# Kernel optimization log

Hardware: AMD Instinct MI355X
Metric: run time of the kernel (lower is better)

Reference implementation:

```python
import jax, jax.numpy as jnp
import numpy as np

NEG = -1e9  # stands in for -inf in masked_fill; identical softmax output, grad-safe


def _sfu(inputs, fusion, Wr, Wg):
    # SFU: m = [x, f, x*f, x-f]; o = relu(m@Wr)*g + (1-g)*x, g = sigmoid(m@Wg)
    m = jnp.concatenate([inputs, fusion, inputs * fusion, inputs - fusion], axis=-1)
    x = jax.nn.relu(m @ Wr)
    g = jax.nn.sigmoid(m @ Wg)
    return x * g + (1.0 - g) * inputs


def _stage(U, V, cmask, qmask, E, B, p):
    # One Aligner stage = InterAlign followed by SelfAlign. Batch-first layout (b, len, d).
    Wu, bu, Wv, bv, Wri, Wgi, gi, W1, b1, W2, b2, Wrs, Wgs, gs = p
    # ---- InterAlign ----
    Ct = jax.nn.relu(U @ Wu + bu)              # (b, c, d)
    Qt = jax.nn.relu(V @ Wv + bv)              # (b, q, d)
    E0 = jnp.einsum('bcd,bqd->bcq', Ct, Qt)    # (b, c, q)
    if E is not None:
        Es = jax.nn.softmax(jnp.where(cmask[:, :, None] == 0, NEG, E), axis=1)   # softmax over c
        Bs = jax.nn.softmax(jnp.where(cmask[:, None, :] == 0, NEG, B), axis=2)   # softmax over c (cols)
        E = E0 + gi * jnp.einsum('bce,beq->bcq', Bs, Es)
    else:
        E = E0
    Ett = jax.nn.softmax(jnp.where(qmask[:, None, :] == 0, NEG, E), axis=2)
    qctx = jnp.einsum('bcq,bqd->bcd', Ett, V)  # attend question
    h = _sfu(U, qctx, Wri, Wgi)
    # ---- SelfAlign ----
    H1 = jax.nn.relu(h @ W1 + b1)
    H2 = jax.nn.relu(h @ W2 + b2)
    B0 = jnp.einsum('bcd,bed->bce', H1, H2)    # (b, c, c)
    if B is not None:
        B1s = jax.nn.softmax(jnp.where(cmask[:, :, None] == 0, NEG, B), axis=1)
        B2s = jax.nn.softmax(jnp.where(cmask[:, None, :] == 0, NEG, B), axis=2)
        B = B0 + gs * jnp.einsum('bce,bef->bcf', B2s, B1s)
    else:
        B = B0
    c = U.shape[1]
    B = B * (1.0 - jnp.eye(c, dtype=B.dtype))[None]  # masked_fill_(eye, 0.0): zero diagonal
    Btt = jax.nn.softmax(jnp.where(cmask[:, None, :] == 0, NEG, B), axis=2)
    hctx = jnp.einsum('bce,bed->bcd', Btt, h)
    Z = _sfu(h, hctx, Wrs, Wgs)
    return Z, E, B


def setup_inputs() -> dict:
    key = jax.random.key(0)
    b, c_len, q_len, d = 8, 768, 96, 768
    T = 2  # number of aligner stages
    ks = jax.random.split(key, 16)
    s = 0.02
    inp = {
        'U': jax.random.normal(ks[0], (b, c_len, d), jnp.float32),
        'V': jax.random.normal(ks[1], (b, q_len, d), jnp.float32),
        'U_mask': jax.random.randint(ks[2], (b, c_len), 0, 2).astype(jnp.int32),
        'V_mask': jax.random.randint(ks[3], (b, q_len), 0, 2).astype(jnp.int32),
        'Wu': jax.random.normal(ks[4], (T, d, d), jnp.float32) * s,
        'bu': jnp.zeros((T, d), jnp.float32),
        'Wv': jax.random.normal(ks[5], (T, d, d), jnp.float32) * s,
        'bv': jnp.zeros((T, d), jnp.float32),
        'Wr_i': jax.random.normal(ks[6], (T, 4 * d, d), jnp.float32) * s,
        'Wg_i': jax.random.normal(ks[7], (T, 4 * d, d), jnp.float32) * s,
        'gamma_i': jnp.full((T,), 3.0, jnp.float32),
        'W1': jax.random.normal(ks[8], (T, d, d), jnp.float32) * s,
        'b1': jnp.zeros((T, d), jnp.float32),
        'W2': jax.random.normal(ks[9], (T, d, d), jnp.float32) * s,
        'b2': jnp.zeros((T, d), jnp.float32),
        'Wr_s': jax.random.normal(ks[10], (T, 4 * d, d), jnp.float32) * s,
        'Wg_s': jax.random.normal(ks[11], (T, 4 * d, d), jnp.float32) * s,
        'gamma_s': jnp.full((T,), 3.0, jnp.float32),
    }
    return inp


def reference(U, V, U_mask, V_mask, Wu, bu, Wv, bv, Wr_i, Wg_i, gamma_i,
              W1, b1, W2, b2, Wr_s, Wg_s, gamma_s):
    E = None
    B = None
    x = U
    for t in range(Wu.shape[0]):  # fixed small stage loop (align_1 -> align_2)
        p = (Wu[t], bu[t], Wv[t], bv[t], Wr_i[t], Wg_i[t], gamma_i[t],
             W1[t], b1[t], W2[t], b2[t], Wr_s[t], Wg_s[t], gamma_s[t])
        x, E, B = _stage(x, V, U_mask, V_mask, E, B, p)
    return x
```

## Files before the change

kernel.cpp:

```cpp
#include <hip/hip_runtime.h>
#include <math.h>

#define NEGV -1e9f

typedef short bf16x8 __attribute__((ext_vector_type(8)));
typedef float f32x4 __attribute__((ext_vector_type(4)));
typedef unsigned short ushort8v __attribute__((ext_vector_type(8)));

static __device__ __forceinline__ unsigned short f2bf(float f) {
  unsigned int u = __float_as_uint(f);
  unsigned int r = (u + 0x7fffu + ((u >> 16) & 1u)) >> 16;
  return (unsigned short)r;
}

static __device__ __forceinline__ int xcd_swz(int lin, int nwg) {
  int q = nwg >> 3, r = nwg & 7;
  int x = lin & 7, i = lin >> 3;
  return (x < r) ? x * (q + 1) + i : r * (q + 1) + (x - r) * q + i;
}

__device__ __forceinline__ float wred_max(float v) {
  #pragma unroll
  for (int o = 32; o > 0; o >>= 1) v = fmaxf(v, __shfl_down(v, o, 64));
  return v;
}
__device__ __forceinline__ float wred_sum(float v) {
  #pragma unroll
  for (int o = 32; o > 0; o >>= 1) v += __shfl_down(v, o, 64);
  return v;
}

__global__ __launch_bounds__(256)
void softmax_row_mask(const float* __restrict__ X, const int* __restrict__ mask,
                      float* __restrict__ Y, unsigned short* __restrict__ Ybf,
                      int R, int Cn)
{
  int bz = blockIdx.y, r = blockIdx.x, tid = threadIdx.x;
  const float* xr = X + ((size_t)bz * R + r) * Cn;
  const int*   mr = mask + (size_t)bz * Cn;
  float*       yr = Y ? (Y + ((size_t)bz * R + r) * Cn) : nullptr;
  unsigned short* yb = Ybf ? (Ybf + ((size_t)bz * R + r) * Cn) : nullptr;
  __shared__ float sred[4];

  float mx = -INFINITY;
  for (int i = tid; i < Cn; i += 256) {
    float v = (mr[i] != 0) ? xr[i] : NEGV;
    mx = fmaxf(mx, v);
  }
  float wm = wred_max(mx);
  if ((tid & 63) == 0) sred[tid >> 6] = wm;
  __syncthreads();
  mx = fmaxf(fmaxf(sred[0], sred[1]), fmaxf(sred[2], sred[3]));
  __syncthreads();

  float s = 0.f;
  for (int i = tid; i < Cn; i += 256) {
    float v = (mr[i] != 0) ? xr[i] : NEGV;
    s += expf(v - mx);
  }
  float wsv = wred_sum(s);
  if ((tid & 63) == 0) sred[tid >> 6] = wsv;
  __syncthreads();
  s = sred[0] + sred[1] + sred[2] + sred[3];
  float inv = 1.0f / s;

  for (int i = tid; i < Cn; i += 256) {
    float v = (mr[i] != 0) ? xr[i] : NEGV;
    float o = expf(v - mx) * inv;
    if (yr) yr[i] = o;
    if (yb) yb[i] = f2bf(o);
  }
}

__global__ __launch_bounds__(256)
void transp_f32(const float* __restrict__ X, float* __restrict__ Y,
                int R, int C, long sX, long sY)
{
  int bz = blockIdx.z;
  X += (size_t)bz * sX;
  Y += (size_t)bz * sY;
  __shared__ float T[64][65];
  int c0 = blockIdx.x * 64, r0 = blockIdx.y * 64;
  int t = threadIdx.x;
  int tr = t >> 4, tc4 = (t & 15) * 4;
  #pragma unroll
  for (int rr = 0; rr < 4; ++rr) {
    int r = tr + rr * 16;
    float4 v = make_float4(0.f, 0.f, 0.f, 0.f);
    if (c0 + tc4 < C)
      v = *reinterpret_cast<const float4*>(X + (size_t)(r0 + r) * C + c0 + tc4);
    T[r][tc4 + 0] = v.x; T[r][tc4 + 1] = v.y;
    T[r][tc4 + 2] = v.z; T[r][tc4 + 3] = v.w;
  }
  __syncthreads();
  #pragma unroll
  for (int rr = 0; rr < 4; ++rr) {
    int cc = tr + rr * 16;
    int gc = c0 + cc;
    if (gc < C) {
      float4 o = make_float4(T[tc4 + 0][cc], T[tc4 + 1][cc], T[tc4 + 2][cc], T[tc4 + 3][cc]);
      *reinterpret_cast<float4*>(Y + (size_t)gc * R + r0 + tc4) = o;
    }
  }
}

__global__ __launch_bounds__(256)
void transpV(const float* __restrict__ V, unsigned short* __restrict__ VT)
{
  int bz = blockIdx.z;
  const float* Vb = V + (size_t)bz * 96 * 768;
  unsigned short* Yb = VT + (size_t)bz * 768 * 96;
  __shared__ float T[64][65];
  int c0 = blockIdx.x * 64, r0 = blockIdx.y * 64;
  int t = threadIdx.x;
  int tr = t >> 4, tc4 = (t & 15) * 4;
  #pragma unroll
  for (int rr = 0; rr < 4; ++rr) {
    int r = tr + rr * 16;
    int gr = r0 + r;
    float4 v = make_float4(0.f, 0.f, 0.f, 0.f);
    if (gr < 96)
      v = *reinterpret_cast<const float4*>(Vb + (size_t)gr * 768 + c0 + tc4);
    T[r][tc4 + 0] = v.x; T[r][tc4 + 1] = v.y;
    T[r][tc4 + 2] = v.z; T[r][tc4 + 3] = v.w;
  }
  __syncthreads();
  #pragma unroll
  for (int rr = 0; rr < 4; ++rr) {
    int cc = tr + rr * 16;
    int gc = c0 + cc;
    #pragma unroll
    for (int e = 0; e < 4; ++e) {
      int gr = r0 + tc4 + e;
      if (gr < 96) Yb[(size_t)gc * 96 + gr] = f2bf(T[tc4 + e][cc]);
    }
  }
}

__global__ __launch_bounds__(256)
void concat_bf16(const float* __restrict__ X, const float* __restrict__ F,
                 unsigned short* __restrict__ Mc)
{
  int idx = blockIdx.x * 256 + threadIdx.x;
  int m  = idx / 96;
  int kk = (idx - m * 96) * 8;
  const float* xp = X + (size_t)m * 768 + kk;
  const float* fp = F + (size_t)m * 768 + kk;
  float4 a0 = *reinterpret_cast<const float4*>(xp);
  float4 a1 = *reinterpret_cast<const float4*>(xp + 4);
  float4 b0 = *reinterpret_cast<const float4*>(fp);
  float4 b1 = *reinterpret_cast<const float4*>(fp + 4);
  float xa[8] = {a0.x, a0.y, a0.z, a0.w, a1.x, a1.y, a1.z, a1.w};
  float fa[8] = {b0.x, b0.y, b0.z, b0.w, b1.x, b1.y, b1.z, b1.w};
  ushort8v o0, o1, o2;
  #pragma unroll
  for (int i = 0; i < 8; ++i) {
    o0[i] = f2bf(xa[i]);
    o1[i] = f2bf(fa[i]);
    o2[i] = f2bf(xa[i] * fa[i]);
  }
  unsigned short* base = Mc + (size_t)m * 2304 + kk;
  *reinterpret_cast<ushort8v*>(base)        = o0;
  *reinterpret_cast<ushort8v*>(base +  768) = o1;
  *reinterpret_cast<ushort8v*>(base + 1536) = o2;
}

__global__ __launch_bounds__(256)
void transp_cast4(const float* __restrict__ W0, const float* __restrict__ W1a,
                  const float* __restrict__ W2a, const float* __restrict__ W3a,
                  unsigned short* __restrict__ Wt)
{
  int z = blockIdx.z;
  const float* W = (z == 0) ? W0 : (z == 1) ? W1a : (z == 2) ? W2a : W3a;
  unsigned short* Y = Wt + (size_t)z * 768 * 768;
  __shared__ float T[64][65];
  int n0 = blockIdx.x * 64, k0 = blockIdx.y * 64;
  int t = threadIdx.x;
  int tr = t >> 4, tc4 = (t & 15) * 4;
  #pragma unroll
  for (int r = 0; r < 4; ++r) {
    int k = tr + r * 16;
    float4 v = *reinterpret_cast<const float4*>(W + (size_t)(k0 + k) * 768 + n0 + tc4);
    T[k][tc4 + 0] = v.x; T[k][tc4 + 1] = v.y; T[k][tc4 + 2] = v.z; T[k][tc4 + 3] = v.w;
  }
  __syncthreads();
  #pragma unroll
  for (int r = 0; r < 4; ++r) {
    int n = tr + r * 16;
    ushort4 o;
    o.x = f2bf(T[tc4 + 0][n]); o.y = f2bf(T[tc4 + 1][n]);
    o.z = f2bf(T[tc4 + 2][n]); o.w = f2bf(T[tc4 + 3][n]);
    *reinterpret_cast<ushort4*>(Y + (size_t)(n0 + n) * 768 + k0 + tc4) = o;
  }
}

__global__ __launch_bounds__(256)
void transp_cast2(const float* __restrict__ Wa, const float* __restrict__ Wb,
                  unsigned short* __restrict__ Wt)
{
  const float* W = blockIdx.z ? Wb : Wa;
  unsigned short* Y = Wt + (size_t)blockIdx.z * 768 * 2304;
  __shared__ float T[64][65];
  int n0 = blockIdx.x * 64, k0 = blockIdx.y * 64;
  int t = threadIdx.x;
  int tr = t >> 4, tc4 = (t & 15) * 4;
  #pragma unroll
  for (int r = 0; r < 4; ++r) {
    int k = tr + r * 16;
    int gk = k0 + k;
    float4 v = *reinterpret_cast<const float4*>(W + (size_t)gk * 768 + n0 + tc4);
    if (gk < 768) {
      float4 u = *reinterpret_cast<const float4*>(W + (size_t)(gk + 2304) * 768 + n0 + tc4);
      v.x += u.x; v.y += u.y; v.z += u.z; v.w += u.w;
    } else if (gk < 1536) {
      float4 u = *reinterpret_cast<const float4*>(W + (size_t)(gk + 1536) * 768 + n0 + tc4);
      v.x -= u.x; v.y -= u.y; v.z -= u.z; v.w -= u.w;
    }
    T[k][tc4 + 0] = v.x; T[k][tc4 + 1] = v.y; T[k][tc4 + 2] = v.z; T[k][tc4 + 3] = v.w;
  }
  __syncthreads();
  #pragma unroll
  for (int r = 0; r < 4; ++r) {
    int n = tr + r * 16;
    ushort4 o;
    o.x = f2bf(T[tc4 + 0][n]); o.y = f2bf(T[tc4 + 1][n]);
    o.z = f2bf(T[tc4 + 2][n]); o.w = f2bf(T[tc4 + 3][n]);
    *reinterpret_cast<ushort4*>(Y + (size_t)(n0 + n) * 2304 + k0 + tc4) = o;
  }
}

__global__ __launch_bounds__(256)
void transp_cast(const float* __restrict__ W, unsigned short* __restrict__ Wt,
                 int K, long sW, long sWt)
{
  int bz = blockIdx.z;
  W  += (size_t)bz * sW;
  Wt += (size_t)bz * sWt;
  __shared__ float T[64][65];
  int n0 = blockIdx.x * 64, k0 = blockIdx.y * 64;
  int t = threadIdx.x;
  int tr = t >> 4, tc4 = (t & 15) * 4;
  #pragma unroll
  for (int r = 0; r < 4; ++r) {
    int k = tr + r * 16;
    float4 v = *reinterpret_cast<const float4*>(W + (size_t)(k0 + k) * 768 + n0 + tc4);
    T[k][tc4 + 0] = v.x; T[k][tc4 + 1] = v.y; T[k][tc4 + 2] = v.z; T[k][tc4 + 3] = v.w;
  }
  __syncthreads();
  #pragma unroll
  for (int r = 0; r < 4; ++r) {
    int n = tr + r * 16;
    ushort4 o;
    o.x = f2bf(T[tc4 + 0][n]); o.y = f2bf(T[tc4 + 1][n]);
    o.z = f2bf(T[tc4 + 2][n]); o.w = f2bf(T[tc4 + 3][n]);
    *reinterpret_cast<ushort4*>(Wt + (size_t)(n0 + n) * K + k0 + tc4) = o;
  }
}

__global__ __launch_bounds__(256)
void cast_bf16(const float* __restrict__ X, unsigned short* __restrict__ Y, int n8)
{
  int idx = blockIdx.x * 256 + threadIdx.x;
  if (idx >= n8) return;
  float4 a0 = *reinterpret_cast<const float4*>(X + (size_t)idx * 8);
  float4 a1 = *reinterpret_cast<const float4*>(X + (size_t)idx * 8 + 4);
  ushort8v o;
  o[0] = f2bf(a0.x); o[1] = f2bf(a0.y); o[2] = f2bf(a0.z); o[3] = f2bf(a0.w);
  o[4] = f2bf(a1.x); o[5] = f2bf(a1.y); o[6] = f2bf(a1.z); o[7] = f2bf(a1.w);
  *reinterpret_cast<ushort8v*>(Y + (size_t)idx * 8) = o;
}


template<int NB, int WAVES>
__global__ __launch_bounds__(64 * WAVES)
void mfma_gemm(const unsigned short* __restrict__ A,
               const unsigned short* __restrict__ Bt0,
               const unsigned short* __restrict__ Bt1,
               const float* __restrict__ bias0, const float* __restrict__ bias1,
               const float* __restrict__ alphap, const float* __restrict__ C0,
               float* __restrict__ F0, float* __restrict__ F1,
               unsigned short* __restrict__ O0, unsigned short* __restrict__ O1,
               int M, int N, int K,
               long sA, long sB, long sC0, long sC,
               int relu, int zerodiag)
{
  const int RG = WAVES / 4;
  const int TM = RG * 48;
  __shared__ unsigned short As[2][TM * 32];
  __shared__ unsigned short Bs0[2][2048];
  __shared__ unsigned short Bs1[2][NB == 2 ? 2048 : 16];

  int nx = gridDim.x, ny = gridDim.y;
  int nwg = nx * ny * gridDim.z;
  int lin = blockIdx.x + nx * (blockIdx.y + ny * blockIdx.z);
  int sw = xcd_swz(lin, nwg);
  int bxi = sw % nx; int rest = sw / nx;
  int byi = rest % ny; int bz = rest / ny;

  A   += (size_t)bz * sA;
  Bt0 += (size_t)bz * sB;
  if (NB == 2) Bt1 += (size_t)bz * sB;
  const float* C0b = C0 ? (C0 + (size_t)bz * sC0) : nullptr;

  int tid = threadIdx.x;
  int w = tid >> 6, l = tid & 63;
  int m0 = byi * TM, n0 = bxi * 64;
  int wr = w >> 2, wc = w & 3;

  int g8 = (((l & 3) ^ ((l >> 3) & 3))) * 8;
  int rowA = w * 16 + (l >> 2); if (rowA > TM - 1) rowA = TM - 1;
  int rB = n0 + (w & 3) * 16 + (l >> 2); if (rB > N - 1) rB = N - 1;
  const unsigned short* srcA  = A + (size_t)(m0 + rowA) * K + g8;
  const unsigned short* srcB0 = Bt0 + (size_t)rB * K + g8;
  const unsigned short* srcB1 = (NB == 2) ? Bt1 + (size_t)rB * K + g8 : nullptr;

#define GG_STAGE(kt, bi) do { int kk0 = (kt) * 32;                                                                        \
    if (w < TM / 16)                                                                                                      \
      __builtin_amdgcn_global_load_lds((const unsigned int*)(srcA + kk0),  (unsigned int*)&As[bi][0]  + w * 256, 16, 0, 0); \
    if (w < 4)                                                                                                            \
      __builtin_amdgcn_global_load_lds((const unsigned int*)(srcB0 + kk0), (unsigned int*)&Bs0[bi][0] + w * 256, 16, 0, 0); \
    if (NB == 2 && w >= 4)                                                                                                \
      __builtin_amdgcn_global_load_lds((const unsigned int*)(srcB1 + kk0), (unsigned int*)&Bs1[bi][0] + (w - 4) * 256, 16, 0, 0); \
  } while (0)

  f32x4 a0[3] = {};
  f32x4 a1v[3] = {};

  const int NT = K / 32;
  int prm = ((l >> 4) ^ ((l >> 1) & 3)) * 8;
  GG_STAGE(0, 0);
  __syncthreads();
  int cur = 0;
  for (int kt = 0; kt < NT; ++kt) {
    if (kt + 1 < NT) GG_STAGE(kt + 1, cur ^ 1);

    bf16x8 af[3];
    #pragma unroll
    for (int i = 0; i < 3; ++i) {
      int off = (wr * 48 + i * 16 + (l & 15)) * 32 + prm;
      af[i] = *reinterpret_cast<const bf16x8*>(&As[cur][off]);
    }
    int offB = (wc * 16 + (l & 15)) * 32 + prm;
    bf16x8 b0 = *reinterpret_cast<const bf16x8*>(&Bs0[cur][offB]);
    #pragma unroll
    for (int i = 0; i < 3; ++i)
      a0[i] = __builtin_amdgcn_mfma_f32_16x16x32_bf16(af[i], b0, a0[i], 0, 0, 0);
    if (NB == 2) {
      bf16x8 b1 = *reinterpret_cast<const bf16x8*>(&Bs1[cur][offB]);
      #pragma unroll
      for (int i = 0; i < 3; ++i)
        a1v[i] = __builtin_amdgcn_mfma_f32_16x16x32_bf16(af[i], b1, a1v[i], 0, 0, 0);
    }
    __syncthreads();
    cur ^= 1;
  }
#undef GG_STAGE

  float alpha = alphap ? alphap[0] : 1.0f;
  float* F0b = F0 ? F0 + (size_t)bz * sC : nullptr;
  float* F1b = F1 ? F1 + (size_t)bz * sC : nullptr;
  unsigned short* O0b = O0 ? O0 + (size_t)bz * sC : nullptr;
  unsigned short* O1b = O1 ? O1 + (size_t)bz * sC : nullptr;

  #pragma unroll
  for (int i = 0; i < 3; ++i) {
    #pragma unroll
    for (int qq = 0; qq < 4; ++qq) {
      int gm = m0 + wr * 48 + i * 16 + (l >> 4) * 4 + qq;
      int gn = n0 + wc * 16 + (l & 15);
      if (gn >= N) continue;
      size_t oidx = (size_t)gm * N + gn;
      float v = alpha * a0[i][qq];
      if (bias0) v += bias0[gn];
      if (relu) v = fmaxf(v, 0.f);
      if (C0b) v += C0b[oidx];
      if (zerodiag && gm == gn) v = 0.f;
      if (F0b) F0b[oidx] = v;
      if (O0b) O0b[oidx] = f2bf(v);
      if (NB == 2) {
        float v1 = alpha * a1v[i][qq];
        if (bias1) v1 += bias1[gn];
        if (relu) v1 = fmaxf(v1, 0.f);
        if (F1b) F1b[oidx] = v1;
        if (O1b) O1b[oidx] = f2bf(v1);
      }
    }
  }
}

__global__ __launch_bounds__(512)
void sfu_mfma(const unsigned short* __restrict__ Mc,
              const unsigned short* __restrict__ Brt,
              const unsigned short* __restrict__ Bgt,
              const float* __restrict__ Xres, float* __restrict__ Z,
              unsigned short* __restrict__ Zb)
{
  __shared__ unsigned short As[2][3072];
  __shared__ unsigned short Brs[2][2048];
  __shared__ unsigned short Bgs[2][2048];
  const int K = 2304;
  const int NT = 72;

  int nx = gridDim.x, ny = gridDim.y;
  int nwg = nx * ny;
  int lin = blockIdx.x + nx * blockIdx.y;
  int sw = xcd_swz(lin, nwg);
  int bxi = sw % nx; int byi = sw / nx;

  int tid = threadIdx.x;
  int w = tid >> 6, l = tid & 63;
  int m0 = byi * 96, n0 = bxi * 64;
  int wr = w >> 2, wc = w & 3;

  int g8 = (((l & 3) ^ ((l >> 3) & 3))) * 8;
  int rowA = w * 16 + (l >> 2); if (rowA > 95) rowA = 95;
  int rB = n0 + (w & 3) * 16 + (l >> 2);
  const unsigned short* srcA = Mc  + (size_t)(m0 + rowA) * K + g8;
  const unsigned short* srcR = Brt + (size_t)rB * K + g8;
  const unsigned short* srcG = Bgt + (size_t)rB * K + g8;

#define SFU_STAGE(kt, bi) do { int kk0 = (kt) * 32;                                                                      \
    if (w < 6)                                                                                                           \
      __builtin_amdgcn_global_load_lds((const unsigned int*)(srcA + kk0), (unsigned int*)&As[bi][0]  + w * 256, 16, 0, 0); \
    if (w < 4)                                                                                                           \
      __builtin_amdgcn_global_load_lds((const unsigned int*)(srcR + kk0), (unsigned int*)&Brs[bi][0] + w * 256, 16, 0, 0); \
    if (w >= 4)                                                                                                          \
      __builtin_amdgcn_global_load_lds((const unsigned int*)(srcG + kk0), (unsigned int*)&Bgs[bi][0] + (w - 4) * 256, 16, 0, 0); \
  } while (0)

  f32x4 aR[3] = {};
  f32x4 aG[3] = {};

  int prm = ((l >> 4) ^ ((l >> 1) & 3)) * 8;
  SFU_STAGE(0, 0);
  __syncthreads();
  int cur = 0;
  for (int kt = 0; kt < NT; ++kt) {
    if (kt + 1 < NT) SFU_STAGE(kt + 1, cur ^ 1);

    bf16x8 af[3];
    #pragma unroll
    for (int i = 0; i < 3; ++i) {
      int off = (wr * 48 + i * 16 + (l & 15)) * 32 + prm;
      af[i] = *reinterpret_cast<const bf16x8*>(&As[cur][off]);
    }
    int offB = (wc * 16 + (l & 15)) * 32 + prm;
    bf16x8 br = *reinterpret_cast<const bf16x8*>(&Brs[cur][offB]);
    bf16x8 bg = *reinterpret_cast<const bf16x8*>(&Bgs[cur][offB]);
    #pragma unroll
    for (int i = 0; i < 3; ++i) {
      aR[i] = __builtin_amdgcn_mfma_f32_16x16x32_bf16(af[i], br, aR[i], 0, 0, 0);
      aG[i] = __builtin_amdgcn_mfma_f32_16x16x32_bf16(af[i], bg, aG[i], 0, 0, 0);
    }
    __syncthreads();
    cur ^= 1;
  }
#undef SFU_STAGE

  #pragma unroll
  for (int i = 0; i < 3; ++i) {
    #pragma unroll
    for (int qq = 0; qq < 4; ++qq) {
      int gm = m0 + wr * 48 + i * 16 + (l >> 4) * 4 + qq;
      int gn = n0 + wc * 16 + (l & 15);
      float r = fmaxf(aR[i][qq], 0.f);
      float g = 1.0f / (1.0f + expf(-aG[i][qq]));
      float xv = Xres[(size_t)gm * 768 + gn];
      float z = r * g + (1.0f - g) * xv;
      Z[(size_t)gm * 768 + gn] = z;
      if (Zb) Zb[(size_t)gm * 768 + gn] = f2bf(z);
    }
  }
}

static void launch_mfma1(const unsigned short* A, const unsigned short* Bt,
                         const float* bias, const float* alphap, const float* C0,
                         float* F0, unsigned short* O0,
                         int M, int N, int K, long sA, long sB, long sC0, long sC,
                         int relu, int zd, int batch, int tm, hipStream_t s)
{
  dim3 g((N + 63) / 64, M / tm, batch);
  if (tm == 48)
    mfma_gemm<1, 4><<<g, 256, 0, s>>>(A, Bt, nullptr, bias, nullptr, alphap, C0,
                                      F0, nullptr, O0, nullptr, M, N, K, sA, sB, sC0, sC, relu, zd);
  else
    mfma_gemm<1, 8><<<g, 512, 0, s>>>(A, Bt, nullptr, bias, nullptr, alphap, C0,
                                      F0, nullptr, O0, nullptr, M, N, K, sA, sB, sC0, sC, relu, zd);
}

static void launch_mfma2(const unsigned short* A, const unsigned short* Bt0,
                         const unsigned short* Bt1, const float* bias0, const float* bias1,
                         unsigned short* O0, unsigned short* O1,
                         int M, int N, int K, long sA, long sB,
                         int relu, int batch, hipStream_t s)
{
  dim3 g((N + 63) / 64, M / 96, batch);
  mfma_gemm<2, 8><<<g, 512, 0, s>>>(A, Bt0, Bt1, bias0, bias1, nullptr, nullptr,
                                    nullptr, nullptr, O0, O1, M, N, K, sA, sB, 0, sA,
                                    relu, 0);
}

static void launch_sfu(const float* x, const float* f, const float* Wr, const float* Wg,
                       const float* xres, float* z, unsigned short* zb,
                       unsigned short* Mc, unsigned short* Wt, hipStream_t s)
{
  concat_bf16<<<dim3(2304), 256, 0, s>>>(x, f, Mc);
  unsigned short* Wrt = Wt;
  unsigned short* Wgt = Wt + (size_t)768 * 2304;
  transp_cast2<<<dim3(12, 36, 2), 256, 0, s>>>(Wr, Wg, Wt);
  sfu_mfma<<<dim3(12, 64), 512, 0, s>>>(Mc, Wrt, Wgt, xres, z, zb);
}

extern "C" void kernel_launch(void* const* d_in, const int* in_sizes, int n_in,
                              void* d_out, int out_size, void* d_ws, size_t ws_size,
                              hipStream_t stream)
{
  const int b = 8, c = 768, q = 96, d = 768, T = 2;
  const float* U   = (const float*)d_in[0];
  const float* V   = (const float*)d_in[1];
  const int*   Um  = (const int*)d_in[2];
  const int*   Vm  = (const int*)d_in[3];
  const float* Wu  = (const float*)d_in[4];
  const float* bu  = (const float*)d_in[5];
  const float* Wv  = (const float*)d_in[6];
  const float* bv  = (const float*)d_in[7];
  const float* Wri = (const float*)d_in[8];
  const float* Wgi = (const float*)d_in[9];
  const float* gi  = (const float*)d_in[10];
  const float* W1  = (const float*)d_in[11];
  const float* b1  = (const float*)d_in[12];
  const float* W2  = (const float*)d_in[13];
  const float* b2  = (const float*)d_in[14];
  const float* Wrs = (const float*)d_in[15];
  const float* Wgs = (const float*)d_in[16];
  const float* gs  = (const float*)d_in[17];
  float* out = (float*)d_out;

  const size_t big = (size_t)b * c * d;
  const size_t smE = (size_t)b * c * q;
  float* ws   = (float*)d_ws;
  float* xbuf = ws + 0 * big;
  float* h    = ws + 1 * big;
  float* Bm   = ws + 2 * big;
  float* t1   = ws + 3 * big;
  float* t2   = ws + 4 * big;
  float* t3   = ws + 5 * big;
  float* t4   = ws + 6 * big;
  float* Ebuf = ws + 7 * big;
  float* E0b  = Ebuf + smE;
  float* Esb  = E0b + smE;
  float* spare = Esb + smE;
  float* slotE = spare + smE;
  float* WTf  = slotE + big / 2;

  unsigned short* Mc  = (unsigned short*)t1;
  unsigned short* Wt  = (unsigned short*)t4;
  unsigned short* t1h = (unsigned short*)t1;
  unsigned short* t3h = (unsigned short*)t3;
  unsigned short* t3h2 = t3h + big;
  unsigned short* slotEb = (unsigned short*)slotE;
  unsigned short* H1b = t1h;
  unsigned short* H2b = H1b + big;
  unsigned short* WuT = (unsigned short*)WTf;
  unsigned short* WvT  = WuT  + (size_t)d * d;
  unsigned short* W1T  = WvT  + (size_t)d * d;
  unsigned short* W2T  = W1T  + (size_t)d * d;
  unsigned short* Vb16 = W2T  + (size_t)d * d;
  unsigned short* Qtbb = Vb16 + smE;
  unsigned short* VTb  = Qtbb + smE;
  unsigned short* EsTb = VTb  + smE;
  unsigned short* Ettb = EsTb + smE;

  const long cd = (long)c * d, cq = (long)c * q, qd = (long)q * d, cc = (long)c * c;
  const size_t dd = (size_t)d * d;
  const int cast_big = (int)(big / 8);
  (void)ws_size; (void)spare;

  const float* x = U;
  for (int t = 0; t < T; ++t) {
    const float* Writ = Wri + (size_t)t * 4 * dd;
    const float* Wgit = Wgi + (size_t)t * 4 * dd;
    const float* Wrst = Wrs + (size_t)t * 4 * dd;
    const float* Wgst = Wgs + (size_t)t * 4 * dd;

    transp_cast4<<<dim3(12, 12, 4), 256, 0, stream>>>(Wu + t * dd, Wv + t * dd,
                                                      W1 + t * dd, W2 + t * dd, WuT);
    if (t == 0) {
      cast_bf16<<<dim3((int)(smE / 8 / 256)), 256, 0, stream>>>(V, Vb16, (int)(smE / 8));
      transpV<<<dim3(12, 2, b), 256, 0, stream>>>(V, VTb);
      cast_bf16<<<dim3(cast_big / 256), 256, 0, stream>>>(x, t3h, cast_big);
    }

    launch_mfma1(t3h, WuT, bu + t * d, nullptr, nullptr, nullptr, t1h,
                 b * c, d, d, 0, 0, 0, 0, 1, 0, 1, 96, stream);
    launch_mfma1(Vb16, WvT, bv + t * d, nullptr, nullptr, nullptr, Qtbb,
                 b * q, d, d, 0, 0, 0, 0, 1, 0, 1, 48, stream);
    float* e0dst = (t == 0) ? Ebuf : E0b;
    launch_mfma1(t1h, Qtbb, nullptr, nullptr, nullptr, e0dst, nullptr,
                 c, q, d, cd, qd, 0, cq, 0, 0, b, 48, stream);
    if (t > 0) {
      transp_f32<<<dim3(2, 12, b), 256, 0, stream>>>(Ebuf, Esb, c, q, cq, cq);
      softmax_row_mask<<<dim3(q, b), 256, 0, stream>>>(Esb, Um, nullptr, EsTb, q, c);
      softmax_row_mask<<<dim3(c, b), 256, 0, stream>>>(Bm, Um, nullptr, slotEb, c, c);
      launch_mfma1(slotEb, EsTb, nullptr, gi + t, E0b, Ebuf, nullptr,
                   c, q, c, cc, cq, cq, cq, 0, 0, b, 48, stream);
    }
    softmax_row_mask<<<dim3(c, b), 256, 0, stream>>>(Ebuf, Vm, nullptr, Ettb, c, q);
    launch_mfma1(Ettb, VTb, nullptr, nullptr, nullptr, t4, nullptr,
                 c, d, q, cq, qd, 0, cd, 0, 0, b, 96, stream);
    launch_sfu(x, t4, Writ, Wgit, x, h, t3h, Mc, Wt, stream);
    launch_mfma2(t3h, W1T, W2T, b1 + t * d, b2 + t * d, H1b, H2b,
                 b * c, d, d, 0, 0, 1, 1, stream);
    if (t == 0) {
      launch_mfma1(H1b, H2b, nullptr, nullptr, nullptr, Bm, nullptr,
                   c, c, d, cd, cd, 0, cc, 0, 1, b, 96, stream);
    } else {
      launch_mfma1(H1b, H2b, nullptr, nullptr, nullptr, xbuf, nullptr,
                   c, c, d, cd, cd, 0, cc, 0, 0, b, 96, stream);
      transp_f32<<<dim3(12, 12, b), 256, 0, stream>>>(Bm, t1, c, c, cc, cc);
      softmax_row_mask<<<dim3(c, b), 256, 0, stream>>>(t1, Um, nullptr, t3h2, c, c);
      launch_mfma1(slotEb, t3h2, nullptr, gs + t, xbuf, Bm, nullptr,
                   c, c, c, cc, cc, cc, cc, 0, 1, b, 96, stream);
    }
    softmax_row_mask<<<dim3(c, b), 256, 0, stream>>>(Bm, Um, nullptr, t3h2, c, c);
    transp_cast<<<dim3(12, 12, b), 256, 0, stream>>>(h, slotEb, 768, cd, cd);
    launch_mfma1(t3h2, slotEb, nullptr, nullptr, nullptr, t4, nullptr,
                 c, d, c, cc, cd, 0, cd, 0, 0, b, 96, stream);
    float* zdst = (t == T - 1) ? out : xbuf;
    unsigned short* zb16 = (t == T - 1) ? nullptr : t3h;
    launch_sfu(h, t4, Wrst, Wgst, h, zdst, zb16, Mc, Wt, stream);

    x = xbuf;
  }
}
```

Baseline: 755.0 us.

## Split K across two wave groups with larger per-wave tiles and LDS reduction

In the 8-wave GEMM and SFU kernels, the waves form two groups that take alternating K tiles. Each wave now computes a 48x32 sub-tile instead of 48x16, so every A fragment feeds more MFMAs and fewer LDS reads are needed per MFMA. After the loop the partial sums from group 1 are reduced into group 0 through an LDS buffer, and group 0 writes the epilogue. The cost is more accumulator registers, extra LDS, extra barriers for the reduction, and each wave sitting idle on every other K step. The 4-wave GEMM path is split into its own specialized kernel with unchanged logic.

Measured after the change: 920.6 us. +21.9%, slower.

```diff
diff --git a/kernel.cpp b/kernel.cpp
--- a/kernel.cpp
+++ b/kernel.cpp
@@ -271,24 +271,23 @@
 }
 
 
-template<int NB, int WAVES>
-__global__ __launch_bounds__(64 * WAVES)
-void mfma_gemm(const unsigned short* __restrict__ A,
-               const unsigned short* __restrict__ Bt0,
-               const unsigned short* __restrict__ Bt1,
-               const float* __restrict__ bias0, const float* __restrict__ bias1,
-               const float* __restrict__ alphap, const float* __restrict__ C0,
-               float* __restrict__ F0, float* __restrict__ F1,
-               unsigned short* __restrict__ O0, unsigned short* __restrict__ O1,
-               int M, int N, int K,
-               long sA, long sB, long sC0, long sC,
-               int relu, int zerodiag)
-{
-  const int RG = WAVES / 4;
-  const int TM = RG * 48;
-  __shared__ unsigned short As[2][TM * 32];
+template<int NB>
+__global__ __launch_bounds__(512)
+void mfma_gemm8(const unsigned short* __restrict__ A,
+                const unsigned short* __restrict__ Bt0,
+                const unsigned short* __restrict__ Bt1,
+                const float* __restrict__ bias0, const float* __restrict__ bias1,
+                const float* __restrict__ alphap, const float* __restrict__ C0,
+                float* __restrict__ F0, float* __restrict__ F1,
+                unsigned short* __restrict__ O0, unsigned short* __restrict__ O1,
+                int M, int N, int K,
+                long sA, long sB, long sC0, long sC,
+                int relu, int zerodiag)
+{
+  __shared__ unsigned short As[2][3072];
   __shared__ unsigned short Bs0[2][2048];
   __shared__ unsigned short Bs1[2][NB == 2 ? 2048 : 16];
+  __shared__ float MP[12 * 256];
 
   int nx = gridDim.x, ny = gridDim.y;
   int nwg = nx * ny * gridDim.z;
@@ -304,18 +303,19 @@
 
   int tid = threadIdx.x;
   int w = tid >> 6, l = tid & 63;
-  int m0 = byi * TM, n0 = bxi * 64;
-  int wr = w >> 2, wc = w & 3;
+  int m0 = byi * 96, n0 = bxi * 64;
+  int grp = w >> 2, pos = w & 3;
+  int wr = pos >> 1, wc = pos & 1;
 
   int g8 = (((l & 3) ^ ((l >> 3) & 3))) * 8;
-  int rowA = w * 16 + (l >> 2); if (rowA > TM - 1) rowA = TM - 1;
+  int rowA = w * 16 + (l >> 2); if (rowA > 95) rowA = 95;
   int rB = n0 + (w & 3) * 16 + (l >> 2); if (rB > N - 1) rB = N - 1;
   const unsigned short* srcA  = A + (size_t)(m0 + rowA) * K + g8;
   const unsigned short* srcB0 = Bt0 + (size_t)rB * K + g8;
   const unsigned short* srcB1 = (NB == 2) ? Bt1 + (size_t)rB * K + g8 : nullptr;
 
 #define GG_STAGE(kt, bi) do { int kk0 = (kt) * 32;                                                                        \
-    if (w < TM / 16)                                                                                                      \
+    if (w < 6)                                                                                                            \
       __builtin_amdgcn_global_load_lds((const unsigned int*)(srcA + kk0),  (unsigned int*)&As[bi][0]  + w * 256, 16, 0, 0); \
     if (w < 4)                                                                                                            \
       __builtin_amdgcn_global_load_lds((const unsigned int*)(srcB0 + kk0), (unsigned int*)&Bs0[bi][0] + w * 256, 16, 0, 0); \
@@ -323,8 +323,8 @@
       __builtin_amdgcn_global_load_lds((const unsigned int*)(srcB1 + kk0), (unsigned int*)&Bs1[bi][0] + (w - 4) * 256, 16, 0, 0); \
   } while (0)
 
-  f32x4 a0[3] = {};
-  f32x4 a1v[3] = {};
+  f32x4 a0[2][3] = {};
+  f32x4 a1[2][3] = {};
 
   const int NT = K / 32;
   int prm = ((l >> 4) ^ ((l >> 1) & 3)) * 8;
@@ -334,10 +334,147 @@
   for (int kt = 0; kt < NT; ++kt) {
     if (kt + 1 < NT) GG_STAGE(kt + 1, cur ^ 1);
 
+    if ((kt & 1) == grp) {
+      bf16x8 af[3];
+      #pragma unroll
+      for (int i = 0; i < 3; ++i) {
+        int off = (wr * 48 + i * 16 + (l & 15)) * 32 + prm;
+        af[i] = *reinterpret_cast<const bf16x8*>(&As[cur][off]);
+      }
+      #pragma unroll
+      for (int j = 0; j < 2; ++j) {
+        int offB = (wc * 32 + j * 16 + (l & 15)) * 32 + prm;
+        bf16x8 b0 = *reinterpret_cast<const bf16x8*>(&Bs0[cur][offB]);
+        #pragma unroll
+        for (int i = 0; i < 3; ++i)
+          a0[j][i] = __builtin_amdgcn_mfma_f32_16x16x32_bf16(af[i], b0, a0[j][i], 0, 0, 0);
+        if (NB == 2) {
+          bf16x8 b1 = *reinterpret_cast<const bf16x8*>(&Bs1[cur][offB]);
+          #pragma unroll
+          for (int i = 0; i < 3; ++i)
+            a1[j][i] = __builtin_amdgcn_mfma_f32_16x16x32_bf16(af[i], b1, a1[j][i], 0, 0, 0);
+        }
+      }
+    }
+    __syncthreads();
+    cur ^= 1;
+  }
+#undef GG_STAGE
+
+  int slot = pos * 64 + l;
+  #pragma unroll
+  for (int rnd = 0; rnd < 2 * NB; ++rnd) {
+    f32x4* col = (rnd < 2) ? &a0[rnd][0] : &a1[rnd - 2][0];
+    if (grp == 1) {
+      #pragma unroll
+      for (int i = 0; i < 3; ++i)
+        #pragma unroll
+        for (int k = 0; k < 4; ++k)
+          MP[(i * 4 + k) * 256 + slot] = col[i][k];
+    }
+    __syncthreads();
+    if (grp == 0) {
+      #pragma unroll
+      for (int i = 0; i < 3; ++i)
+        #pragma unroll
+        for (int k = 0; k < 4; ++k)
+          col[i][k] += MP[(i * 4 + k) * 256 + slot];
+    }
+    __syncthreads();
+  }
+
+  if (grp != 0) return;
+
+  float alpha = alphap ? alphap[0] : 1.0f;
+  float* F0b = F0 ? F0 + (size_t)bz * sC : nullptr;
+  float* F1b = F1 ? F1 + (size_t)bz * sC : nullptr;
+  unsigned short* O0b = O0 ? O0 + (size_t)bz * sC : nullptr;
+  unsigned short* O1b = O1 ? O1 + (size_t)bz * sC : nullptr;
+
+  #pragma unroll
+  for (int j = 0; j < 2; ++j) {
+    #pragma unroll
+    for (int i = 0; i < 3; ++i) {
+      #pragma unroll
+      for (int qq = 0; qq < 4; ++qq) {
+        int gm = m0 + wr * 48 + i * 16 + (l >> 4) * 4 + qq;
+        int gn = n0 + wc * 32 + j * 16 + (l & 15);
+        if (gn >= N) continue;
+        size_t oidx = (size_t)gm * N + gn;
+        float v = alpha * a0[j][i][qq];
+        if (bias0) v += bias0[gn];
+        if (relu) v = fmaxf(v, 0.f);
+        if (C0b) v += C0b[oidx];
+        if (zerodiag && gm == gn) v = 0.f;
+        if (F0b) F0b[oidx] = v;
+        if (O0b) O0b[oidx] = f2bf(v);
+        if (NB == 2) {
+          float v1 = alpha * a1[j][i][qq];
+          if (bias1) v1 += bias1[gn];
+          if (relu) v1 = fmaxf(v1, 0.f);
+          if (F1b) F1b[oidx] = v1;
+          if (O1b) O1b[oidx] = f2bf(v1);
+        }
+      }
+    }
+  }
+}
+
+__global__ __launch_bounds__(256)
+void mfma_gemm4(const unsigned short* __restrict__ A,
+                const unsigned short* __restrict__ Bt0,
+                const float* __restrict__ bias0,
+                const float* __restrict__ alphap, const float* __restrict__ C0,
+                float* __restrict__ F0, unsigned short* __restrict__ O0,
+                int M, int N, int K,
+                long sA, long sB, long sC0, long sC,
+                int relu, int zerodiag)
+{
+  __shared__ unsigned short As[2][1536];
+  __shared__ unsigned short Bs0[2][2048];
+
+  int nx = gridDim.x, ny = gridDim.y;
+  int nwg = nx * ny * gridDim.z;
+  int lin = blockIdx.x + nx * (blockIdx.y + ny * blockIdx.z);
+  int sw = xcd_swz(lin, nwg);
+  int bxi = sw % nx; int rest = sw / nx;
+  int byi = rest % ny; int bz = rest / ny;
+
+  A   += (size_t)bz * sA;
+  Bt0 += (size_t)bz * sB;
+  const float* C0b = C0 ? (C0 + (size_t)bz * sC0) : nullptr;
+
+  int tid = threadIdx.x;
+  int w = tid >> 6, l = tid & 63;
+  int m0 = byi * 48, n0 = bxi * 64;
+  int wc = w & 3;
+
+  int g8 = (((l & 3) ^ ((l >> 3) & 3))) * 8;
+  int rowA = w * 16 + (l >> 2); if (rowA > 47) rowA = 47;
+  int rB = n0 + (w & 3) * 16 + (l >> 2); if (rB > N - 1) rB = N - 1;
+  const unsigned short* srcA  = A + (size_t)(m0 + rowA) * K + g8;
+  const unsigned short* srcB0 = Bt0 + (size_t)rB * K + g8;
+
+#define G4_STAGE(kt, bi) do { int kk0 = (kt) * 32;                                                                        \
+    if (w < 3)                                                                                                            \
+      __builtin_amdgcn_global_load_lds((const unsigned int*)(srcA + kk0),  (unsigned int*)&As[bi][0]  + w * 256, 16, 0, 0); \
+    __builtin_amdgcn_global_load_lds((const unsigned int*)(srcB0 + kk0), (unsigned int*)&Bs0[bi][0] + w * 256, 16, 0, 0);   \
+  } while (0)
+
+  f32x4 a0[3] = {};
+
+  const int NT = K / 32;
+  int prm = ((l >> 4) ^ ((l >> 1) & 3)) * 8;
+  G4_STAGE(0, 0);
+  __syncthreads();
+  int cur = 0;
+  for (int kt = 0; kt < NT; ++kt) {
+    if (kt + 1 < NT) G4_STAGE(kt + 1, cur ^ 1);
+
     bf16x8 af[3];
     #pragma unroll
     for (int i = 0; i < 3; ++i) {
-      int off = (wr * 48 + i * 16 + (l & 15)) * 32 + prm;
+      int off = (i * 16 + (l & 15)) * 32 + prm;
       af[i] = *reinterpret_cast<const bf16x8*>(&As[cur][off]);
     }
     int offB = (wc * 16 + (l & 15)) * 32 + prm;
@@ -345,28 +482,20 @@
     #pragma unroll
     for (int i = 0; i < 3; ++i)
       a0[i] = __builtin_amdgcn_mfma_f32_16x16x32_bf16(af[i], b0, a0[i], 0, 0, 0);
-    if (NB == 2) {
-      bf16x8 b1 = *reinterpret_cast<const bf16x8*>(&Bs1[cur][offB]);
-      #pragma unroll
-      for (int i = 0; i < 3; ++i)
-        a1v[i] = __builtin_amdgcn_mfma_f32_16x16x32_bf16(af[i], b1, a1v[i], 0, 0, 0);
-    }
     __syncthreads();
     cur ^= 1;
   }
-#undef GG_STAGE
+#undef G4_STAGE
 
   float alpha = alphap ? alphap[0] : 1.0f;
   float* F0b = F0 ? F0 + (size_t)bz * sC : nullptr;
-  float* F1b = F1 ? F1 + (size_t)bz * sC : nullptr;
   unsigned short* O0b = O0 ? O0 + (size_t)bz * sC : nullptr;
-  unsigned short* O1b = O1 ? O1 + (size_t)bz * sC : nullptr;
 
   #pragma unroll
   for (int i = 0; i < 3; ++i) {
     #pragma unroll
     for (int qq = 0; qq < 4; ++qq) {
-      int gm = m0 + wr * 48 + i * 16 + (l >> 4) * 4 + qq;
+      int gm = m0 + i * 16 + (l >> 4) * 4 + qq;
       int gn = n0 + wc * 16 + (l & 15);
       if (gn >= N) continue;
       size_t oidx = (size_t)gm * N + gn;
@@ -377,13 +506,6 @@
       if (zerodiag && gm == gn) v = 0.f;
       if (F0b) F0b[oidx] = v;
       if (O0b) O0b[oidx] = f2bf(v);
-      if (NB == 2) {
-        float v1 = alpha * a1v[i][qq];
-        if (bias1) v1 += bias1[gn];
-        if (relu) v1 = fmaxf(v1, 0.f);
-        if (F1b) F1b[oidx] = v1;
-        if (O1b) O1b[oidx] = f2bf(v1);
-      }
     }
   }
 }
@@ -398,6 +520,7 @@
   __shared__ unsigned short As[2][3072];
   __shared__ unsigned short Brs[2][2048];
   __shared__ unsigned short Bgs[2][2048];
+  __shared__ float MP[12 * 256];
   const int K = 2304;
   const int NT = 72;
 
@@ -410,7 +533,8 @@
   int tid = threadIdx.x;
   int w = tid >> 6, l = tid & 63;
   int m0 = byi * 96, n0 = bxi * 64;
-  int wr = w >> 2, wc = w & 3;
+  int grp = w >> 2, pos = w & 3;
+  int wr = pos >> 1, wc = pos & 1;
 
   int g8 = (((l & 3) ^ ((l >> 3) & 3))) * 8;
   int rowA = w * 16 + (l >> 2); if (rowA > 95) rowA = 95;
@@ -428,8 +552,8 @@
       __builtin_amdgcn_global_load_lds((const unsigned int*)(srcG + kk0), (unsigned int*)&Bgs[bi][0] + (w - 4) * 256, 16, 0, 0); \
   } while (0)
 
-  f32x4 aR[3] = {};
-  f32x4 aG[3] = {};
+  f32x4 aR[2][3] = {};
+  f32x4 aG[2][3] = {};
 
   int prm = ((l >> 4) ^ ((l >> 1) & 3)) * 8;
   SFU_STAGE(0, 0);
@@ -438,37 +562,69 @@
   for (int kt = 0; kt < NT; ++kt) {
     if (kt + 1 < NT) SFU_STAGE(kt + 1, cur ^ 1);
 
-    bf16x8 af[3];
+    if ((kt & 1) == grp) {
+      bf16x8 af[3];
+      #pragma unroll
+      for (int i = 0; i < 3; ++i) {
+        int off = (wr * 48 + i * 16 + (l & 15)) * 32 + prm;
+        af[i] = *reinterpret_cast<const bf16x8*>(&As[cur][off]);
+      }
+      #pragma unroll
+      for (int j = 0; j < 2; ++j) {
+        int offB = (wc * 32 + j * 16 + (l & 15)) * 32 + prm;
+        bf16x8 br = *reinterpret_cast<const bf16x8*>(&Brs[cur][offB]);
+        bf16x8 bg = *reinterpret_cast<const bf16x8*>(&Bgs[cur][offB]);
+        #pragma unroll
+        for (int i = 0; i < 3; ++i) {
+          aR[j][i] = __builtin_amdgcn_mfma_f32_16x16x32_bf16(af[i], br, aR[j][i], 0, 0, 0);
+          aG[j][i] = __builtin_amdgcn_mfma_f32_16x16x32_bf16(af[i], bg, aG[j][i], 0, 0, 0);
+        }
+      }
+    }
+    __syncthreads();
+    cur ^= 1;
+  }
+#undef SFU_STAGE
+
+  int slot = pos * 64 + l;
+  #pragma unroll
+  for (int rnd = 0; rnd < 4; ++rnd) {
+    f32x4* col = (rnd < 2) ? &aR[rnd][0] : &aG[rnd - 2][0];
+    if (grp == 1) {
+      #pragma unroll
+      for (int i = 0; i < 3; ++i)
+        #pragma unroll
+        for (int k = 0; k < 4; ++k)
+          MP[(i * 4 + k) * 256 + slot] = col[i][k];
+    }
+    __syncthreads();
+    if (grp == 0) {
+      #pragma unroll
+      for (int i = 0; i < 3; ++i)
+        #pragma unroll
+        for (int k = 0; k < 4; ++k)
+          col[i][k] += MP[(i * 4 + k) * 256 + slot];
+    }
+    __syncthreads();
+  }
+
+  if (grp != 0) return;
+
+  #pragma unroll
+  for (int j = 0; j < 2; ++j) {
     #pragma unroll
     for (int i = 0; i < 3; ++i) {
-      int off = (wr * 48 + i * 16 + (l & 15)) * 32 + prm;
-      af[i] = *reinterpret_cast<const bf16x8*>(&As[cur][off]);
-    }
-    int offB = (wc * 16 + (l & 15)) * 32 + prm;
-    bf16x8 br = *reinterpret_cast<const bf16x8*>(&Brs[cur][offB]);
-    bf16x8 bg = *reinterpret_cast<const bf16x8*>(&Bgs[cur][offB]);
-    #pragma unroll
-    for (int i = 0; i < 3; ++i) {
-      aR[i] = __builtin_amdgcn_mfma_f32_16x16x32_bf16(af[i], br, aR[i], 0, 0, 0);
-      aG[i] = __builtin_amdgcn_mfma_f32_16x16x32_bf16(af[i], bg, aG[i], 0, 0, 0);
-    }
-    __syncthreads();
-    cur ^= 1;
-  }
-#undef SFU_STAGE
-
-  #pragma unroll
-  for (int i = 0; i < 3; ++i) {
-    #pragma unroll
-    for (int qq = 0; qq < 4; ++qq) {
-      int gm = m0 + wr * 48 + i * 16 + (l >> 4) * 4 + qq;
-      int gn = n0 + wc * 16 + (l & 15);
-      float r = fmaxf(aR[i][qq], 0.f);
-      float g = 1.0f / (1.0f + expf(-aG[i][qq]));
-      float xv = Xres[(size_t)gm * 768 + gn];
-      float z = r * g + (1.0f - g) * xv;
-      Z[(size_t)gm * 768 + gn] = z;
-      if (Zb) Zb[(size_t)gm * 768 + gn] = f2bf(z);
+      #pragma unroll
+      for (int qq = 0; qq < 4; ++qq) {
+        int gm = m0 + wr * 48 + i * 16 + (l >> 4) * 4 + qq;
+        int gn = n0 + wc * 32 + j * 16 + (l & 15);
+        float r = fmaxf(aR[j][i][qq], 0.f);
+        float g = 1.0f / (1.0f + expf(-aG[j][i][qq]));
+        float xv = Xres[(size_t)gm * 768 + gn];
+        float z = r * g + (1.0f - g) * xv;
+        Z[(size_t)gm * 768 + gn] = z;
+        if (Zb) Zb[(size_t)gm * 768 + gn] = f2bf(z);
+      }
     }
   }
 }
@@ -481,11 +637,11 @@
 {
   dim3 g((N + 63) / 64, M / tm, batch);
   if (tm == 48)
-    mfma_gemm<1, 4><<<g, 256, 0, s>>>(A, Bt, nullptr, bias, nullptr, alphap, C0,
-                                      F0, nullptr, O0, nullptr, M, N, K, sA, sB, sC0, sC, relu, zd);
+    mfma_gemm4<<<g, 256, 0, s>>>(A, Bt, bias, alphap, C0, F0, O0,
+                                 M, N, K, sA, sB, sC0, sC, relu, zd);
   else
-    mfma_gemm<1, 8><<<g, 512, 0, s>>>(A, Bt, nullptr, bias, nullptr, alphap, C0,
-                                      F0, nullptr, O0, nullptr, M, N, K, sA, sB, sC0, sC, relu, zd);
+    mfma_gemm8<1><<<g, 512, 0, s>>>(A, Bt, nullptr, bias, nullptr, alphap, C0,
+                                    F0, nullptr, O0, nullptr, M, N, K, sA, sB, sC0, sC, relu, zd);
 }
 
 static void launch_mfma2(const unsigned short* A, const unsigned short* Bt0,
@@ -495,9 +651,9 @@
                          int relu, int batch, hipStream_t s)
 {
   dim3 g((N + 63) / 64, M / 96, batch);
-  mfma_gemm<2, 8><<<g, 512, 0, s>>>(A, Bt0, Bt1, bias0, bias1, nullptr, nullptr,
-                                    nullptr, nullptr, O0, O1, M, N, K, sA, sB, 0, sA,
-                                    relu, 0);
+  mfma_gemm8<2><<<g, 512, 0, s>>>(A, Bt0, Bt1, bias0, bias1, nullptr, nullptr,
+                                  nullptr, nullptr, O0, O1, M, N, K, sA, sB, 0, sA,
+                                  relu, 0);
 }
 
 static void launch_sfu(const float* x, const float* f, const float* Wr, const float* Wg,
```

## Use online softmax in row kernel and fuse transpose with column softmax

Applied to the files above, without the earlier changes.

The row softmax kernel now computes the running max and sum in a single pass with online rescaling, dropping one read pass over each row. A new kernel fuses the f32 transpose with the masked column softmax on the c×c B matrix, writing transposed bf16 output directly and removing the intermediate f32 transpose buffer round trip. The fused kernel launches only 12×b blocks, which may underuse the GPU, and it reads the input twice with extra exp work for the online rescaling.

After: 770.7 us. +2.1%, slower.

```diff
diff --git a/kernel.cpp b/kernel.cpp
--- a/kernel.cpp
+++ b/kernel.cpp
@@ -40,35 +40,110 @@
   const int*   mr = mask + (size_t)bz * Cn;
   float*       yr = Y ? (Y + ((size_t)bz * R + r) * Cn) : nullptr;
   unsigned short* yb = Ybf ? (Ybf + ((size_t)bz * R + r) * Cn) : nullptr;
-  __shared__ float sred[4];
-
-  float mx = -INFINITY;
+  __shared__ float sred[4], sred2[4];
+
+  float m = -INFINITY, s = 0.f;
   for (int i = tid; i < Cn; i += 256) {
     float v = (mr[i] != 0) ? xr[i] : NEGV;
-    mx = fmaxf(mx, v);
-  }
-  float wm = wred_max(mx);
+    float nm = fmaxf(m, v);
+    s = s * expf(m - nm) + expf(v - nm);
+    m = nm;
+  }
+  float wm = wred_max(m);
   if ((tid & 63) == 0) sred[tid >> 6] = wm;
   __syncthreads();
-  mx = fmaxf(fmaxf(sred[0], sred[1]), fmaxf(sred[2], sred[3]));
-  __syncthreads();
-
-  float s = 0.f;
+  float fm = fmaxf(fmaxf(sred[0], sred[1]), fmaxf(sred[2], sred[3]));
+  float sadj = s * expf(m - fm);
+  float wsv = wred_sum(sadj);
+  if ((tid & 63) == 0) sred2[tid >> 6] = wsv;
+  __syncthreads();
+  float fs = sred2[0] + sred2[1] + sred2[2] + sred2[3];
+  float inv = 1.0f / fs;
+
   for (int i = tid; i < Cn; i += 256) {
     float v = (mr[i] != 0) ? xr[i] : NEGV;
-    s += expf(v - mx);
-  }
-  float wsv = wred_sum(s);
-  if ((tid & 63) == 0) sred[tid >> 6] = wsv;
-  __syncthreads();
-  s = sred[0] + sred[1] + sred[2] + sred[3];
-  float inv = 1.0f / s;
-
-  for (int i = tid; i < Cn; i += 256) {
-    float v = (mr[i] != 0) ? xr[i] : NEGV;
-    float o = expf(v - mx) * inv;
+    float o = expf(v - fm) * inv;
     if (yr) yr[i] = o;
     if (yb) yb[i] = f2bf(o);
+  }
+}
+
+__global__ __launch_bounds__(256)
+void colsoftmax_T(const float* __restrict__ X, const int* __restrict__ mask,
+                  unsigned short* __restrict__ Y, int n)
+{
+  int bz = blockIdx.y;
+  const float* Xb = X + (size_t)bz * n * n;
+  const int*   mr = mask + (size_t)bz * n;
+  unsigned short* Yb = Y + (size_t)bz * n * n;
+  __shared__ float T[64][65];
+  __shared__ float rm[4][64], rs[4][64];
+  __shared__ float sm[64], sinv[64];
+  int j0 = blockIdx.x * 64;
+  int t = threadIdx.x;
+  int tr = t >> 4, tc4 = (t & 15) * 4;
+  int jj = t & 63, qq = t >> 6;
+  const int NTile = n / 64;
+
+  float m = -INFINITY, s = 0.f;
+  for (int it = 0; it < NTile; ++it) {
+    int i0 = it * 64;
+    __syncthreads();
+    #pragma unroll
+    for (int r = 0; r < 4; ++r) {
+      int i = tr + r * 16;
+      float4 v = *reinterpret_cast<const float4*>(Xb + (size_t)(i0 + i) * n + j0 + tc4);
+      int mk = mr[i0 + i];
+      T[i][tc4 + 0] = mk ? v.x : NEGV;
+      T[i][tc4 + 1] = mk ? v.y : NEGV;
+      T[i][tc4 + 2] = mk ? v.z : NEGV;
+      T[i][tc4 + 3] = mk ? v.w : NEGV;
+    }
+    __syncthreads();
+    #pragma unroll
+    for (int r = 0; r < 16; ++r) {
+      float v = T[qq * 16 + r][jj];
+      float nm = fmaxf(m, v);
+      s = s * expf(m - nm) + expf(v - nm);
+      m = nm;
+    }
+  }
+  rm[qq][jj] = m; rs[qq][jj] = s;
+  __syncthreads();
+  if (t < 64) {
+    float m0 = rm[0][t], m1 = rm[1][t], m2 = rm[2][t], m3 = rm[3][t];
+    float fm = fmaxf(fmaxf(m0, m1), fmaxf(m2, m3));
+    float fs = rs[0][t] * expf(m0 - fm) + rs[1][t] * expf(m1 - fm)
+             + rs[2][t] * expf(m2 - fm) + rs[3][t] * expf(m3 - fm);
+    sm[t] = fm; sinv[t] = 1.0f / fs;
+  }
+  __syncthreads();
+
+  for (int it = 0; it < NTile; ++it) {
+    int i0 = it * 64;
+    __syncthreads();
+    #pragma unroll
+    for (int r = 0; r < 4; ++r) {
+      int i = tr + r * 16;
+      float4 v = *reinterpret_cast<const float4*>(Xb + (size_t)(i0 + i) * n + j0 + tc4);
+      int mk = mr[i0 + i];
+      T[i][tc4 + 0] = mk ? v.x : NEGV;
+      T[i][tc4 + 1] = mk ? v.y : NEGV;
+      T[i][tc4 + 2] = mk ? v.z : NEGV;
+      T[i][tc4 + 3] = mk ? v.w : NEGV;
+    }
+    __syncthreads();
+    #pragma unroll
+    for (int r = 0; r < 4; ++r) {
+      int jr = tr + r * 16;
+      float fm = sm[jr], inv = sinv[jr];
+      ushort4 o;
+      o.x = f2bf(expf(T[tc4 + 0][jr] - fm) * inv);
+      o.y = f2bf(expf(T[tc4 + 1][jr] - fm) * inv);
+      o.z = f2bf(expf(T[tc4 + 2][jr] - fm) * inv);
+      o.w = f2bf(expf(T[tc4 + 3][jr] - fm) * inv);
+      *reinterpret_cast<ushort4*>(Yb + (size_t)(j0 + jr) * n + i0 + tc4) = o;
+    }
   }
 }
 
@@ -617,8 +692,7 @@
     } else {
       launch_mfma1(H1b, H2b, nullptr, nullptr, nullptr, xbuf, nullptr,
                    c, c, d, cd, cd, 0, cc, 0, 0, b, 96, stream);
-      transp_f32<<<dim3(12, 12, b), 256, 0, stream>>>(Bm, t1, c, c, cc, cc);
-      softmax_row_mask<<<dim3(c, b), 256, 0, stream>>>(t1, Um, nullptr, t3h2, c, c);
+      colsoftmax_T<<<dim3(12, b), 256, 0, stream>>>(Bm, Um, t3h2, c);
       launch_mfma1(slotEb, t3h2, nullptr, gs + t, xbuf, Bm, nullptr,
                    c, c, c, cc, cc, cc, cc, 0, 1, b, 96, stream);
     }
```
